# Kernel tuning notes

Measured on AMD Instinct MI355X. Metric: run time of the kernel, lower is better.

Reference implementation:

```python
import jax, jax.numpy as jnp
import numpy as np

B, T, E = 4, 2048, 768
HN, HS = 12, 64          # head_num, head_size = E // HN
L = 6                    # n_layer
FF = 4 * E
O = 1                    # output_dim
EPS = 1e-5


def setup_inputs() -> dict:
    key = jax.random.key(0)
    ks = iter(jax.random.split(key, 40))
    r = lambda shape, s=0.02: jax.random.normal(next(ks), shape, jnp.float32) * s
    inp = {
        'idx': jax.random.normal(next(ks), (B, T, E), jnp.float32),
        'hidden': jnp.zeros((1, B, E), jnp.float32),
        # per-layer, per-head q/k/v linears
        'wq': r((L, HN, E, HS)), 'bq': jnp.zeros((L, HN, HS), jnp.float32),
        'wk': r((L, HN, E, HS)), 'bk': jnp.zeros((L, HN, HS), jnp.float32),
        'wv': r((L, HN, E, HS)), 'bv': jnp.zeros((L, HN, HS), jnp.float32),
        'wproj': r((L, E, E)), 'bproj': jnp.zeros((L, E), jnp.float32),
        'ln1_g': jnp.ones((L, E), jnp.float32), 'ln1_b': jnp.zeros((L, E), jnp.float32),
        'ln2_g': jnp.ones((L, E), jnp.float32), 'ln2_b': jnp.zeros((L, E), jnp.float32),
        'w1': r((L, E, FF)), 'b1': jnp.zeros((L, FF), jnp.float32),
        'w2': r((L, FF, E)), 'b2': jnp.zeros((L, E), jnp.float32),
        'lnf_g': jnp.ones((E,), jnp.float32), 'lnf_b': jnp.zeros((E,), jnp.float32),
        'fw1': r((E, FF)), 'fb1': jnp.zeros((FF,), jnp.float32),
        'fw2': r((FF, E)), 'fb2': jnp.zeros((E,), jnp.float32),
        'hw': r((E, O)), 'hb': jnp.zeros((O,), jnp.float32),
    }
    return inp


def _layernorm(x, g, b):
    m = jnp.mean(x, axis=-1, keepdims=True)
    v = jnp.var(x, axis=-1, keepdims=True)
    return (x - m) * jax.lax.rsqrt(v + EPS) * g + b


def _forward(idx, wq, bq, wk, bk, wv, bv, wproj, bproj,
             ln1_g, ln1_b, ln2_g, ln2_b, w1, b1, w2, b2,
             lnf_g, lnf_b, fw1, fb1, fw2, fb2, hw, hb):
    x = idx
    Bn, Tn, En = x.shape
    causal = jnp.tril(jnp.ones((Tn, Tn), bool))  # [T,T]
    scale = 1.0 / jnp.sqrt(jnp.asarray(En, x.dtype))  # NOTE: divides by sqrt(n_embed), as in source
    for l in range(wq.shape[0]):
        h = _layernorm(x, ln1_g[l], ln1_b[l])
        q = jnp.einsum('bte,hes->bhts', h, wq[l]) + bq[l][None, :, None, :]
        k = jnp.einsum('bte,hes->bhts', h, wk[l]) + bk[l][None, :, None, :]
        v = jnp.einsum('bte,hes->bhts', h, wv[l]) + bv[l][None, :, None, :]
        scores = jnp.einsum('bhts,bhus->bhtu', q, k) * scale
        scores = jnp.where(causal, scores, -jnp.inf)
        att = jax.nn.softmax(scores, axis=-1)
        o = jnp.einsum('bhtu,bhus->bhts', att, v)          # [B,HN,T,HS]
        o = o.transpose(0, 2, 1, 3).reshape(Bn, Tn, En)     # concat heads
        x = x + o @ wproj[l] + bproj[l]
        h = _layernorm(x, ln2_g[l], ln2_b[l])
        ff = jax.nn.gelu(h @ w1[l] + b1[l], approximate=False) @ w2[l] + b2[l]
        x = x + ff
    x = _layernorm(x, lnf_g, lnf_b)
    x = jax.nn.gelu(x @ fw1 + fb1, approximate=False) @ fw2 + fb2
    logits = x @ hw + hb            # [B,T,O]
    logits = logits[-1]             # [T,O]  (source: logits[-1,:,:])
    return jnp.squeeze(logits, axis=-1)  # [T]


def reference(idx, hidden, wq, bq, wk, bk, wv, bv, wproj, bproj,
              ln1_g, ln1_b, ln2_g, ln2_b, w1, b1, w2, b2,
              lnf_g, lnf_b, fw1, fb1, fw2, fb2, hw, hb):
    # hidden is accepted but unused by the original module.
    del hidden
    return _forward(idx, wq, bq, wk, bk, wv, bv, wproj, bproj,
                    ln1_g, ln1_b, ln2_g, ln2_b, w1, b1, w2, b2,
                    lnf_g, lnf_b, fw1, fb1, fw2, fb2, hw, hb)
```

## Files before the change

### kernel.cpp

```cpp
#include <hip/hip_runtime.h>
#include <math.h>

#define TT 2048
#define EE 768
#define HNN 12
#define HSS 64
#define NLAYER 6
#define FFD 3072
#define QKVN 2304

constexpr float LN_EPS = 1e-5f;
constexpr float ATT_SCALE = 0.03608439182435161f;
constexpr float ATT_SCALE_L2E = 0.03608439182435161f * 1.4426950408889634f;

typedef __attribute__((ext_vector_type(8))) short bf16x8;
typedef __attribute__((ext_vector_type(4))) float f32x4;

__device__ __forceinline__ ushort f2bf(float f) {
    union { float f; uint u; } c; c.f = f;
    const uint u = c.u;
    return (ushort)((u + 0x7fffu + ((u >> 16) & 1u)) >> 16);
}

__device__ __forceinline__ void gload16(const void* g, void* l) {
    __builtin_amdgcn_global_load_lds((const __attribute__((address_space(1))) void*)g,
                                     (__attribute__((address_space(3))) void*)l, 16, 0, 0);
}

__global__ __launch_bounds__(256) void copy4_kernel(float4* __restrict__ dst,
                                                    const float4* __restrict__ src, int n4) {
    int i = blockIdx.x * 256 + threadIdx.x;
    if (i < n4) dst[i] = src[i];
}

__global__ __launch_bounds__(256) void ln_kernel(const float* __restrict__ in,
                                                 const float* __restrict__ g,
                                                 const float* __restrict__ b,
                                                 ushort* __restrict__ out) {
    __shared__ float red[8];
    const int t = blockIdx.x;
    const int tid = threadIdx.x;
    const float* row = in + (size_t)t * EE;
    float v0 = row[tid], v1 = row[tid + 256], v2 = row[tid + 512];
    float s = v0 + v1 + v2;
#pragma unroll
    for (int m = 1; m < 64; m <<= 1) s += __shfl_xor(s, m, 64);
    if ((tid & 63) == 0) red[tid >> 6] = s;
    __syncthreads();
    const float mean = (red[0] + red[1] + red[2] + red[3]) * (1.0f / EE);
    const float d0 = v0 - mean, d1 = v1 - mean, d2 = v2 - mean;
    float qq = d0 * d0 + d1 * d1 + d2 * d2;
#pragma unroll
    for (int m = 1; m < 64; m <<= 1) qq += __shfl_xor(qq, m, 64);
    __syncthreads();
    if ((tid & 63) == 0) red[tid >> 6] = qq;
    __syncthreads();
    const float var = (red[0] + red[1] + red[2] + red[3]) * (1.0f / EE);
    const float rstd = rsqrtf(var + LN_EPS);
    ushort* orow = out + (size_t)t * EE;
    orow[tid]       = f2bf(d0 * rstd * g[tid]       + b[tid]);
    orow[tid + 256] = f2bf(d1 * rstd * g[tid + 256] + b[tid + 256]);
    orow[tid + 512] = f2bf(d2 * rstd * g[tid + 512] + b[tid + 512]);
}

__device__ __forceinline__ void transpose64(const float* __restrict__ src, int sld,
                                            ushort* __restrict__ dst, int dld,
                                            int k0, int n0, int tid) {
    __shared__ float t[64][68];
#pragma unroll
    for (int p = 0; p < 4; p++) {
        const int kr = p * 16 + (tid >> 4);
        *(float4*)&t[kr][(tid & 15) * 4] =
            *(const float4*)&src[(size_t)(k0 + kr) * sld + n0 + (tid & 15) * 4];
    }
    __syncthreads();
#pragma unroll
    for (int q = 0; q < 2; q++) {
        const int nl = q * 32 + (tid >> 3);
        const int kc = (tid & 7) * 8;
        ushort v[8];
#pragma unroll
        for (int j = 0; j < 8; j++) v[j] = f2bf(t[kc + j][nl]);
        uint4 o;
        o.x = (uint)v[0] | ((uint)v[1] << 16);
        o.y = (uint)v[2] | ((uint)v[3] << 16);
        o.z = (uint)v[4] | ((uint)v[5] << 16);
        o.w = (uint)v[6] | ((uint)v[7] << 16);
        *(uint4*)&dst[(size_t)(n0 + nl) * dld + k0 + kc] = o;
    }
}

__global__ __launch_bounds__(256) void pack_t_kernel(const float* __restrict__ src, int sld,
                                                     ushort* __restrict__ dst, int dld) {
    transpose64(src, sld, dst, dld, blockIdx.x * 64, blockIdx.y * 64, threadIdx.x);
}

__global__ __launch_bounds__(256) void pack_qkv_kernel(const float* __restrict__ wq,
                                                       const float* __restrict__ wk,
                                                       const float* __restrict__ wv,
                                                       ushort* __restrict__ dst) {
    const int z = blockIdx.z;
    const int which = z / HNN, hd = z % HNN;
    const float* src = (which == 0 ? wq : which == 1 ? wk : wv) + (size_t)hd * EE * HSS;
    ushort* d = dst + (size_t)(which * EE + hd * HSS) * EE;
    transpose64(src, HSS, d, EE, blockIdx.x * 64, 0, threadIdx.x);
}

__global__ __launch_bounds__(256) void vtrans_kernel(const ushort* __restrict__ qkv,
                                                     ushort* __restrict__ vT) {
    const int t = blockIdx.x * 256 + threadIdx.x;
    const int d = t & 63;
    const int rest = t >> 6;
    const int tb = rest & 255;
    const int hd = rest >> 8;
    const ushort* src = qkv + 1536 + hd * 64 + d;
    ushort v[8];
#pragma unroll
    for (int j = 0; j < 8; j++) v[j] = src[(size_t)(tb * 8 + j) * QKVN];
    uint4 o;
    o.x = (uint)v[0] | ((uint)v[1] << 16);
    o.y = (uint)v[2] | ((uint)v[3] << 16);
    o.z = (uint)v[4] | ((uint)v[5] << 16);
    o.w = (uint)v[6] | ((uint)v[7] << 16);
    *(uint4*)&vT[((size_t)hd * 64 + d) * TT + tb * 8] = o;
}

template <int EPI>
__global__ __launch_bounds__(256) void gemm_bf16(const ushort* __restrict__ A,
                                                 const ushort* __restrict__ Bt,
                                                 const float* __restrict__ b0,
                                                 const float* __restrict__ b1,
                                                 const float* __restrict__ b2,
                                                 float* __restrict__ outF,
                                                 ushort* __restrict__ outB,
                                                 int N, int K,
                                                 int nby, int KS, int Kslice) {
    __shared__ ushort Al[2][64 * 32];
    __shared__ ushort Bl[2][128 * 32];
    const int tid = threadIdx.x;
    const int wave = tid >> 6, lane = tid & 63;
    const int l15 = lane & 15, q4 = lane >> 4;

    const int nwg = gridDim.x;
    const int wgid = ((int)blockIdx.x & 7) * (nwg >> 3) + ((int)blockIdx.x >> 3);
    const int mb = wgid % nby;
    const int t2 = wgid / nby;
    const int ks = t2 % KS;
    const int nb = t2 / KS;
    const int m0 = mb * 64, n0 = nb * 128;
    const int kbase = ks * Kslice;

    const int srow = lane >> 2;
    const int scb = (lane & 3) ^ ((lane >> 3) & 3);
    const ushort* Ag  = A + (size_t)(m0 + wave * 16 + srow) * K + kbase + scb * 8;
    const ushort* Bg0 = Bt + (size_t)(n0 + wave * 32 + srow) * K + kbase + scb * 8;
    const ushort* Bg1 = Bg0 + (size_t)16 * K;

    auto stage = [&](int buf, int kk) {
        const int off = kk * 32;
        gload16(Ag + off, &Al[buf][(wave * 16) * 32]);
        gload16(Bg0 + off, &Bl[buf][(wave * 32) * 32]);
        gload16(Bg1 + off, &Bl[buf][(wave * 32 + 16) * 32]);
    };

    f32x4 acc[4][2];
#pragma unroll
    for (int i = 0; i < 4; i++)
#pragma unroll
        for (int j = 0; j < 2; j++) acc[i][j] = (f32x4){0.f, 0.f, 0.f, 0.f};

    stage(0, 0);
    __syncthreads();

    const int niter = Kslice >> 5;
    const int cq = (q4 ^ ((l15 >> 1) & 3)) * 8;

    for (int i = 0; i < niter; i++) {
        const int buf = i & 1;
        if (i + 1 < niter) stage(buf ^ 1, i + 1);
        bf16x8 af[4], bfr[2];
#pragma unroll
        for (int ii = 0; ii < 4; ii++)
            af[ii] = *(const bf16x8*)&Al[buf][(ii * 16 + l15) * 32 + cq];
#pragma unroll
        for (int j = 0; j < 2; j++)
            bfr[j] = *(const bf16x8*)&Bl[buf][(wave * 32 + j * 16 + l15) * 32 + cq];
#pragma unroll
        for (int ii = 0; ii < 4; ii++)
#pragma unroll
            for (int j = 0; j < 2; j++)
                acc[ii][j] = __builtin_amdgcn_mfma_f32_16x16x32_bf16(af[ii], bfr[j], acc[ii][j], 0, 0, 0);
        __syncthreads();
    }

#pragma unroll
    for (int i = 0; i < 4; i++) {
        const int row = m0 + i * 16 + q4 * 4;
#pragma unroll
        for (int j = 0; j < 2; j++) {
            const int col = n0 + wave * 32 + j * 16 + l15;
            float bias;
            if constexpr (EPI == 0)
                bias = (col < 768) ? b0[col] : (col < 1536 ? b1[col - 768] : b2[col - 1536]);
            else
                bias = (EPI == 1 && ks != 0) ? 0.f : b0[col];
#pragma unroll
            for (int r = 0; r < 4; r++) {
                const float v = acc[i][j][r] + bias;
                const size_t idx = (size_t)(row + r) * N + col;
                if constexpr (EPI == 0) {
                    outB[idx] = f2bf(v);
                } else if constexpr (EPI == 1) {
                    atomicAdd(&outF[idx], v);
                } else if constexpr (EPI == 2) {
                    outB[idx] = f2bf(0.5f * v * (1.0f + erff(v * 0.70710678118654752f)));
                } else {
                    outF[idx] = v;
                }
            }
        }
    }
}

__global__ __launch_bounds__(256, 2) void attn_mfma(const ushort* __restrict__ qkv,
                                                    const ushort* __restrict__ vT,
                                                    ushort* __restrict__ o_bf) {
    __shared__ __align__(16) uint  Ps[4][16 * 36];
    __shared__ __align__(16) float Po[4][16 * 64];
    __shared__ float Pm[4][16];
    __shared__ float Pl[4][16];

    const int tid = threadIdx.x;
    const int wave = tid >> 6, lane = tid & 63;
    const int l15 = lane & 15, q4 = lane >> 4;

    const int x = (int)blockIdx.x & 7, r = (int)blockIdx.x >> 3;
    int head, qi;
    if (r < 128) { head = x;            qi = 127 - r; }
    else         { head = 8 + (x >> 1); qi = 2 * (191 - r) + (x & 1); }
    const int nkt = (qi >> 2) + 1;
    const int per = (nkt + 3) >> 2;
    const int kt0 = wave * per;
    const int kt1 = min(kt0 + per, nkt);
    const int qrow_g = qi * 16 + l15;

    const ushort* qp = qkv + (size_t)qrow_g * QKVN + head * 64;
    const bf16x8 qa0 = *(const bf16x8*)&qp[q4 * 8];
    const bf16x8 qa1 = *(const bf16x8*)&qp[32 + q4 * 8];

    const ushort* kbase = qkv + 768 + head * 64 + (size_t)l15 * QKVN + q4 * 8;
    const ushort* vbase = vT + ((size_t)head * 64 + l15) * TT + q4 * 8;

    float m_i = -1e30f, l_i = 0.f;
    f32x4 oacc[4];
#pragma unroll
    for (int n = 0; n < 4; n++) oacc[n] = (f32x4){0.f, 0.f, 0.f, 0.f};

    uint* psrow = &Ps[wave][l15 * 36];

    if (kt0 < kt1) {
        bf16x8 kA[8], kB[8], vC[8];
        {
            const ushort* kp = kbase + (size_t)kt0 * 64 * QKVN;
#pragma unroll
            for (int n = 0; n < 4; n++)
#pragma unroll
                for (int kb = 0; kb < 2; kb++)
                    kA[n * 2 + kb] = *(const bf16x8*)(kp + (size_t)(n * 16) * QKVN + kb * 32);
        }

        auto body = [&](bf16x8* kc, bf16x8* kn, int kt) {
            const ushort* vp = vbase + kt * 64;
#pragma unroll
            for (int n = 0; n < 4; n++)
#pragma unroll
                for (int kb = 0; kb < 2; kb++)
                    vC[n * 2 + kb] = *(const bf16x8*)(vp + (size_t)(n * 16) * TT + kb * 32);
            if (kt + 1 < kt1) {
                const ushort* kp = kbase + (size_t)(kt + 1) * 64 * QKVN;
#pragma unroll
                for (int n = 0; n < 4; n++)
#pragma unroll
                    for (int kb = 0; kb < 2; kb++)
                        kn[n * 2 + kb] = *(const bf16x8*)(kp + (size_t)(n * 16) * QKVN + kb * 32);
            }
            f32x4 s[4];
#pragma unroll
            for (int n = 0; n < 4; n++) {
                f32x4 a = (f32x4){0.f, 0.f, 0.f, 0.f};
                a = __builtin_amdgcn_mfma_f32_16x16x32_bf16(kc[n * 2], qa0, a, 0, 0, 0);
                a = __builtin_amdgcn_mfma_f32_16x16x32_bf16(kc[n * 2 + 1], qa1, a, 0, 0, 0);
                s[n] = a;
            }
            float pe[16];
            const bool diag = (kt == nkt - 1);
#pragma unroll
            for (int n = 0; n < 4; n++) {
                const int k0 = kt * 64 + n * 16 + q4 * 4;
#pragma unroll
                for (int rr = 0; rr < 4; rr++) {
                    float xv = s[n][rr] * ATT_SCALE_L2E;
                    if (diag && (k0 + rr) > qrow_g) xv = -1e30f;
                    pe[n * 4 + rr] = xv;
                }
            }
            float t8[8];
#pragma unroll
            for (int i = 0; i < 8; i++) t8[i] = fmaxf(pe[i], pe[i + 8]);
            float mx = fmaxf(fmaxf(fmaxf(t8[0], t8[4]), fmaxf(t8[1], t8[5])),
                             fmaxf(fmaxf(t8[2], t8[6]), fmaxf(t8[3], t8[7])));
            mx = fmaxf(mx, __shfl_xor(mx, 16, 64));
            mx = fmaxf(mx, __shfl_xor(mx, 32, 64));
            const float nm = fmaxf(m_i, mx);
            const float al = exp2f(m_i - nm);
#pragma unroll
            for (int i = 0; i < 16; i++) pe[i] = exp2f(pe[i] - nm);
            float s8[8];
#pragma unroll
            for (int i = 0; i < 8; i++) s8[i] = pe[i] + pe[i + 8];
            float rs = ((s8[0] + s8[4]) + (s8[1] + s8[5])) + ((s8[2] + s8[6]) + (s8[3] + s8[7]));
            rs += __shfl_xor(rs, 16, 64);
            rs += __shfl_xor(rs, 32, 64);
            l_i = l_i * al + rs;
            m_i = nm;
            float alr[4];
#pragma unroll
            for (int rr = 0; rr < 4; rr++) alr[rr] = __shfl(al, q4 * 4 + rr, 64);
#pragma unroll
            for (int n = 0; n < 4; n++) {
                oacc[n][0] *= alr[0];
                oacc[n][1] *= alr[1];
                oacc[n][2] *= alr[2];
                oacc[n][3] *= alr[3];
            }
#pragma unroll
            for (int n = 0; n < 4; n++) {
                uint2 d2;
                d2.x = (uint)f2bf(pe[n * 4 + 0]) | ((uint)f2bf(pe[n * 4 + 1]) << 16);
                d2.y = (uint)f2bf(pe[n * 4 + 2]) | ((uint)f2bf(pe[n * 4 + 3]) << 16);
                *(uint2*)&psrow[(8 * n + 2 * q4 + 4 * l15) & 31] = d2;
            }
            const bf16x8 pa0 = *(const bf16x8*)&psrow[(4 * q4 + 4 * l15) & 31];
            const bf16x8 pa1 = *(const bf16x8*)&psrow[(16 + 4 * q4 + 4 * l15) & 31];
#pragma unroll
            for (int n = 0; n < 4; n++) {
                oacc[n] = __builtin_amdgcn_mfma_f32_16x16x32_bf16(pa0, vC[n * 2], oacc[n], 0, 0, 0);
                oacc[n] = __builtin_amdgcn_mfma_f32_16x16x32_bf16(pa1, vC[n * 2 + 1], oacc[n], 0, 0, 0);
            }
        };

        int kt = kt0;
        for (;;) {
            body(kA, kB, kt);
            if (++kt >= kt1) break;
            body(kB, kA, kt);
            if (++kt >= kt1) break;
        }
    }

#pragma unroll
    for (int n = 0; n < 4; n++)
#pragma unroll
        for (int rr = 0; rr < 4; rr++)
            Po[wave][(q4 * 4 + rr) * 64 + n * 16 + l15] = oacc[n][rr];
    if (q4 == 0) {
        Pm[wave][l15] = m_i;
        Pl[wave][l15] = l_i;
    }
    __syncthreads();

    const int row = tid >> 4;
    const int c4 = (tid & 15) * 4;
    const float m0 = Pm[0][row], m1 = Pm[1][row], m2 = Pm[2][row], m3 = Pm[3][row];
    const float M = fmaxf(fmaxf(m0, m1), fmaxf(m2, m3));
    const float w0 = exp2f(m0 - M), w1 = exp2f(m1 - M), w2 = exp2f(m2 - M), w3 = exp2f(m3 - M);
    const float L = w0 * Pl[0][row] + w1 * Pl[1][row] + w2 * Pl[2][row] + w3 * Pl[3][row];
    const f32x4 o0 = *(const f32x4*)&Po[0][row * 64 + c4];
    const f32x4 o1 = *(const f32x4*)&Po[1][row * 64 + c4];
    const f32x4 o2 = *(const f32x4*)&Po[2][row * 64 + c4];
    const f32x4 o3 = *(const f32x4*)&Po[3][row * 64 + c4];
    const float rl = 1.0f / L;
    uint2 ow;
    {
        const float v0 = (w0 * o0[0] + w1 * o1[0] + w2 * o2[0] + w3 * o3[0]) * rl;
        const float v1 = (w0 * o0[1] + w1 * o1[1] + w2 * o2[1] + w3 * o3[1]) * rl;
        const float v2 = (w0 * o0[2] + w1 * o1[2] + w2 * o2[2] + w3 * o3[2]) * rl;
        const float v3 = (w0 * o0[3] + w1 * o1[3] + w2 * o2[3] + w3 * o3[3]) * rl;
        ow.x = (uint)f2bf(v0) | ((uint)f2bf(v1) << 16);
        ow.y = (uint)f2bf(v2) | ((uint)f2bf(v3) << 16);
    }
    *(uint2*)&o_bf[(size_t)(qi * 16 + row) * EE + head * 64 + c4] = ow;
}

__global__ __launch_bounds__(256) void head_kernel(const float* __restrict__ x,
                                                   const float* __restrict__ hw,
                                                   const float* __restrict__ hb,
                                                   float* __restrict__ out) {
    __shared__ float red[8];
    const int t = blockIdx.x, tid = threadIdx.x;
    const float* row = x + (size_t)t * EE;
    float s = row[tid] * hw[tid] + row[tid + 256] * hw[tid + 256] + row[tid + 512] * hw[tid + 512];
#pragma unroll
    for (int m = 1; m < 64; m <<= 1) s += __shfl_xor(s, m, 64);
    if ((tid & 63) == 0) red[tid >> 6] = s;
    __syncthreads();
    if (tid == 0) out[t] = red[0] + red[1] + red[2] + red[3] + hb[0];
}

extern "C" void kernel_launch(void* const* d_in, const int* in_sizes, int n_in,
                              void* d_out, int out_size, void* d_ws, size_t ws_size,
                              hipStream_t stream) {
    const float* idx   = (const float*)d_in[0];
    const float* wq    = (const float*)d_in[2];
    const float* bq    = (const float*)d_in[3];
    const float* wk    = (const float*)d_in[4];
    const float* bk    = (const float*)d_in[5];
    const float* wv    = (const float*)d_in[6];
    const float* bv    = (const float*)d_in[7];
    const float* wproj = (const float*)d_in[8];
    const float* bproj = (const float*)d_in[9];
    const float* ln1g  = (const float*)d_in[10];
    const float* ln1b  = (const float*)d_in[11];
    const float* ln2g  = (const float*)d_in[12];
    const float* ln2b  = (const float*)d_in[13];
    const float* w1    = (const float*)d_in[14];
    const float* b1    = (const float*)d_in[15];
    const float* w2    = (const float*)d_in[16];
    const float* b2    = (const float*)d_in[17];
    const float* lnfg  = (const float*)d_in[18];
    const float* lnfb  = (const float*)d_in[19];
    const float* fw1   = (const float*)d_in[20];
    const float* fb1   = (const float*)d_in[21];
    const float* fw2   = (const float*)d_in[22];
    const float* fb2   = (const float*)d_in[23];
    const float* hw    = (const float*)d_in[24];
    const float* hb    = (const float*)d_in[25];
    float* out = (float*)d_out;

    char* p = (char*)d_ws;
    auto alloc = [&](size_t bytes) { void* r = (void*)p; p += (bytes + 255) & ~(size_t)255; return r; };
    float*  x     = (float*)alloc((size_t)TT * EE * 4);
    ushort* h_bf  = (ushort*)alloc((size_t)TT * EE * 2);
    ushort* qkvb  = (ushort*)alloc((size_t)TT * QKVN * 2);
    ushort* o_bf  = (ushort*)alloc((size_t)TT * EE * 2);
    ushort* ffb   = (ushort*)alloc((size_t)TT * FFD * 2);
    ushort* Wqkv  = (ushort*)alloc((size_t)QKVN * EE * 2);
    ushort* Wproj = (ushort*)alloc((size_t)EE * EE * 2);
    ushort* W1t   = (ushort*)alloc((size_t)FFD * EE * 2);
    ushort* W2t   = (ushort*)alloc((size_t)EE * FFD * 2);
    ushort* vTb   = (ushort*)alloc((size_t)HNN * HSS * TT * 2);

    copy4_kernel<<<dim3((TT * EE / 4 + 255) / 256), dim3(256), 0, stream>>>(
        (float4*)x, (const float4*)(idx + (size_t)3 * TT * EE), TT * EE / 4);

    for (int l = 0; l < NLAYER; l++) {
        const size_t lw = (size_t)l;
        pack_qkv_kernel<<<dim3(12, 1, 36), dim3(256), 0, stream>>>(
            wq + lw * HNN * EE * HSS, wk + lw * HNN * EE * HSS, wv + lw * HNN * EE * HSS, Wqkv);
        pack_t_kernel<<<dim3(12, 12), dim3(256), 0, stream>>>(wproj + lw * EE * EE, EE, Wproj, EE);
        pack_t_kernel<<<dim3(12, 48), dim3(256), 0, stream>>>(w1 + lw * EE * FFD, FFD, W1t, EE);
        pack_t_kernel<<<dim3(48, 12), dim3(256), 0, stream>>>(w2 + lw * FFD * EE, EE, W2t, FFD);

        ln_kernel<<<dim3(TT), dim3(256), 0, stream>>>(x, ln1g + lw * EE, ln1b + lw * EE, h_bf);
        gemm_bf16<0><<<dim3(576), dim3(256), 0, stream>>>(
            h_bf, Wqkv, bq + lw * EE, bk + lw * EE, bv + lw * EE, nullptr, qkvb,
            QKVN, EE, 32, 1, EE);
        vtrans_kernel<<<dim3(768), dim3(256), 0, stream>>>(qkvb, vTb);
        attn_mfma<<<dim3(1536), dim3(256), 0, stream>>>(qkvb, vTb, o_bf);
        gemm_bf16<1><<<dim3(768), dim3(256), 0, stream>>>(
            o_bf, Wproj, bproj + lw * EE, nullptr, nullptr, x, nullptr,
            EE, EE, 32, 4, 192);
        ln_kernel<<<dim3(TT), dim3(256), 0, stream>>>(x, ln2g + lw * EE, ln2b + lw * EE, h_bf);
        gemm_bf16<2><<<dim3(768), dim3(256), 0, stream>>>(
            h_bf, W1t, b1 + lw * FFD, nullptr, nullptr, nullptr, ffb,
            FFD, EE, 32, 1, EE);
        gemm_bf16<1><<<dim3(768), dim3(256), 0, stream>>>(
            ffb, W2t, b2 + lw * EE, nullptr, nullptr, x, nullptr,
            EE, FFD, 32, 4, 768);
    }

    ln_kernel<<<dim3(TT), dim3(256), 0, stream>>>(x, lnfg, lnfb, h_bf);
    pack_t_kernel<<<dim3(12, 48), dim3(256), 0, stream>>>(fw1, FFD, W1t, EE);
    pack_t_kernel<<<dim3(48, 12), dim3(256), 0, stream>>>(fw2, EE, W2t, FFD);
    gemm_bf16<2><<<dim3(768), dim3(256), 0, stream>>>(
        h_bf, W1t, fb1, nullptr, nullptr, nullptr, ffb, FFD, EE, 32, 1, EE);
    gemm_bf16<3><<<dim3(192), dim3(256), 0, stream>>>(
        ffb, W2t, fb2, nullptr, nullptr, x, nullptr, EE, FFD, 32, 1, FFD);
    head_kernel<<<dim3(TT), dim3(256), 0, stream>>>(x, hw, hb, out);
}
```

Measured before the change: 1.442 ms.

## Assign one query tile per wave in attention, dropping split-KV merge

Attention used to split each 16-row query tile's key range across four waves, then merge their partial softmax states through shared memory after a block barrier. Now each wave owns its own 16-row query tile, and the four waves of a block share the same number of key tiles. That removes the cross-wave merge, the Po/Pm/Pl shared buffers and the __syncthreads, and the grid shrinks from 1536 to 384 blocks. V loads are now prefetched one tile ahead like K, at the cost of more registers. The risks are longer serial loops per wave, lower parallelism (384 blocks of 4 waves), and uncoalesced scalar bf16 output stores.

```diff
diff --git a/kernel.cpp b/kernel.cpp
--- a/kernel.cpp
+++ b/kernel.cpp
@@ -225,23 +225,18 @@
 __global__ __launch_bounds__(256, 2) void attn_mfma(const ushort* __restrict__ qkv,
                                                     const ushort* __restrict__ vT,
                                                     ushort* __restrict__ o_bf) {
-    __shared__ __align__(16) uint  Ps[4][16 * 36];
-    __shared__ __align__(16) float Po[4][16 * 64];
-    __shared__ float Pm[4][16];
-    __shared__ float Pl[4][16];
+    __shared__ __align__(16) uint Ps[4][16 * 36];
 
     const int tid = threadIdx.x;
     const int wave = tid >> 6, lane = tid & 63;
     const int l15 = lane & 15, q4 = lane >> 4;
 
     const int x = (int)blockIdx.x & 7, r = (int)blockIdx.x >> 3;
-    int head, qi;
-    if (r < 128) { head = x;            qi = 127 - r; }
-    else         { head = 8 + (x >> 1); qi = 2 * (191 - r) + (x & 1); }
-    const int nkt = (qi >> 2) + 1;
-    const int per = (nkt + 3) >> 2;
-    const int kt0 = wave * per;
-    const int kt1 = min(kt0 + per, nkt);
+    int head, g;
+    if (r < 32) { head = x;            g = 31 - r; }
+    else        { head = 8 + (x >> 1); g = 2 * (47 - r) + (x & 1); }
+    const int qi = g * 4 + wave;
+    const int nkt = g + 1;
     const int qrow_g = qi * 16 + l15;
 
     const ushort* qp = qkv + (size_t)qrow_g * QKVN + head * 64;
@@ -258,138 +253,109 @@
 
     uint* psrow = &Ps[wave][l15 * 36];
 
-    if (kt0 < kt1) {
-        bf16x8 kA[8], kB[8], vC[8];
-        {
-            const ushort* kp = kbase + (size_t)kt0 * 64 * QKVN;
+    bf16x8 kA[8], kB[8], vA[8], vB[8];
+#pragma unroll
+    for (int n = 0; n < 4; n++)
+#pragma unroll
+        for (int kb = 0; kb < 2; kb++) {
+            kA[n * 2 + kb] = *(const bf16x8*)(kbase + (size_t)(n * 16) * QKVN + kb * 32);
+            vA[n * 2 + kb] = *(const bf16x8*)(vbase + (size_t)(n * 16) * TT + kb * 32);
+        }
+
+    auto body = [&](bf16x8* kc, bf16x8* kn, bf16x8* vc, bf16x8* vn, int kt) {
+        if (kt + 1 < nkt) {
+            const ushort* kp = kbase + (size_t)(kt + 1) * 64 * QKVN;
+            const ushort* vp = vbase + (kt + 1) * 64;
 #pragma unroll
             for (int n = 0; n < 4; n++)
 #pragma unroll
-                for (int kb = 0; kb < 2; kb++)
-                    kA[n * 2 + kb] = *(const bf16x8*)(kp + (size_t)(n * 16) * QKVN + kb * 32);
-        }
-
-        auto body = [&](bf16x8* kc, bf16x8* kn, int kt) {
-            const ushort* vp = vbase + kt * 64;
-#pragma unroll
-            for (int n = 0; n < 4; n++)
-#pragma unroll
-                for (int kb = 0; kb < 2; kb++)
-                    vC[n * 2 + kb] = *(const bf16x8*)(vp + (size_t)(n * 16) * TT + kb * 32);
-            if (kt + 1 < kt1) {
-                const ushort* kp = kbase + (size_t)(kt + 1) * 64 * QKVN;
-#pragma unroll
-                for (int n = 0; n < 4; n++)
-#pragma unroll
-                    for (int kb = 0; kb < 2; kb++)
-                        kn[n * 2 + kb] = *(const bf16x8*)(kp + (size_t)(n * 16) * QKVN + kb * 32);
+                for (int kb = 0; kb < 2; kb++) {
+                    kn[n * 2 + kb] = *(const bf16x8*)(kp + (size_t)(n * 16) * QKVN + kb * 32);
+                    vn[n * 2 + kb] = *(const bf16x8*)(vp + (size_t)(n * 16) * TT + kb * 32);
+                }
+        }
+        f32x4 s[4];
+#pragma unroll
+        for (int n = 0; n < 4; n++) {
+            f32x4 a = (f32x4){0.f, 0.f, 0.f, 0.f};
+            a = __builtin_amdgcn_mfma_f32_16x16x32_bf16(kc[n * 2], qa0, a, 0, 0, 0);
+            a = __builtin_amdgcn_mfma_f32_16x16x32_bf16(kc[n * 2 + 1], qa1, a, 0, 0, 0);
+            s[n] = a;
+        }
+        float pe[16];
+        const bool diag = (kt == nkt - 1);
+#pragma unroll
+        for (int n = 0; n < 4; n++) {
+            const int k0 = kt * 64 + n * 16 + q4 * 4;
+#pragma unroll
+            for (int rr = 0; rr < 4; rr++) {
+                float xv = s[n][rr] * ATT_SCALE_L2E;
+                if (diag && (k0 + rr) > qrow_g) xv = -1e30f;
+                pe[n * 4 + rr] = xv;
             }
-            f32x4 s[4];
-#pragma unroll
-            for (int n = 0; n < 4; n++) {
-                f32x4 a = (f32x4){0.f, 0.f, 0.f, 0.f};
-                a = __builtin_amdgcn_mfma_f32_16x16x32_bf16(kc[n * 2], qa0, a, 0, 0, 0);
-                a = __builtin_amdgcn_mfma_f32_16x16x32_bf16(kc[n * 2 + 1], qa1, a, 0, 0, 0);
-                s[n] = a;
-            }
-            float pe[16];
-            const bool diag = (kt == nkt - 1);
-#pragma unroll
-            for (int n = 0; n < 4; n++) {
-                const int k0 = kt * 64 + n * 16 + q4 * 4;
-#pragma unroll
-                for (int rr = 0; rr < 4; rr++) {
-                    float xv = s[n][rr] * ATT_SCALE_L2E;
-                    if (diag && (k0 + rr) > qrow_g) xv = -1e30f;
-                    pe[n * 4 + rr] = xv;
-                }
-            }
-            float t8[8];
-#pragma unroll
-            for (int i = 0; i < 8; i++) t8[i] = fmaxf(pe[i], pe[i + 8]);
-            float mx = fmaxf(fmaxf(fmaxf(t8[0], t8[4]), fmaxf(t8[1], t8[5])),
-                             fmaxf(fmaxf(t8[2], t8[6]), fmaxf(t8[3], t8[7])));
-            mx = fmaxf(mx, __shfl_xor(mx, 16, 64));
-            mx = fmaxf(mx, __shfl_xor(mx, 32, 64));
-            const float nm = fmaxf(m_i, mx);
-            const float al = exp2f(m_i - nm);
-#pragma unroll
-            for (int i = 0; i < 16; i++) pe[i] = exp2f(pe[i] - nm);
-            float s8[8];
-#pragma unroll
-            for (int i = 0; i < 8; i++) s8[i] = pe[i] + pe[i + 8];
-            float rs = ((s8[0] + s8[4]) + (s8[1] + s8[5])) + ((s8[2] + s8[6]) + (s8[3] + s8[7]));
-            rs += __shfl_xor(rs, 16, 64);
-            rs += __shfl_xor(rs, 32, 64);
-            l_i = l_i * al + rs;
-            m_i = nm;
-            float alr[4];
-#pragma unroll
-            for (int rr = 0; rr < 4; rr++) alr[rr] = __shfl(al, q4 * 4 + rr, 64);
-#pragma unroll
-            for (int n = 0; n < 4; n++) {
-                oacc[n][0] *= alr[0];
-                oacc[n][1] *= alr[1];
-                oacc[n][2] *= alr[2];
-                oacc[n][3] *= alr[3];
-            }
-#pragma unroll
-            for (int n = 0; n < 4; n++) {
-                uint2 d2;
-                d2.x = (uint)f2bf(pe[n * 4 + 0]) | ((uint)f2bf(pe[n * 4 + 1]) << 16);
-                d2.y = (uint)f2bf(pe[n * 4 + 2]) | ((uint)f2bf(pe[n * 4 + 3]) << 16);
-                *(uint2*)&psrow[(8 * n + 2 * q4 + 4 * l15) & 31] = d2;
-            }
-            const bf16x8 pa0 = *(const bf16x8*)&psrow[(4 * q4 + 4 * l15) & 31];
-            const bf16x8 pa1 = *(const bf16x8*)&psrow[(16 + 4 * q4 + 4 * l15) & 31];
-#pragma unroll
-            for (int n = 0; n < 4; n++) {
-                oacc[n] = __builtin_amdgcn_mfma_f32_16x16x32_bf16(pa0, vC[n * 2], oacc[n], 0, 0, 0);
-                oacc[n] = __builtin_amdgcn_mfma_f32_16x16x32_bf16(pa1, vC[n * 2 + 1], oacc[n], 0, 0, 0);
-            }
-        };
-
-        int kt = kt0;
-        for (;;) {
-            body(kA, kB, kt);
-            if (++kt >= kt1) break;
-            body(kB, kA, kt);
-            if (++kt >= kt1) break;
-        }
-    }
-
+        }
+        float t8[8];
+#pragma unroll
+        for (int i = 0; i < 8; i++) t8[i] = fmaxf(pe[i], pe[i + 8]);
+        float mx = fmaxf(fmaxf(fmaxf(t8[0], t8[4]), fmaxf(t8[1], t8[5])),
+                         fmaxf(fmaxf(t8[2], t8[6]), fmaxf(t8[3], t8[7])));
+        mx = fmaxf(mx, __shfl_xor(mx, 16, 64));
+        mx = fmaxf(mx, __shfl_xor(mx, 32, 64));
+        const float nm = fmaxf(m_i, mx);
+        const float al = exp2f(m_i - nm);
+#pragma unroll
+        for (int i = 0; i < 16; i++) pe[i] = exp2f(pe[i] - nm);
+        float s8[8];
+#pragma unroll
+        for (int i = 0; i < 8; i++) s8[i] = pe[i] + pe[i + 8];
+        float rs = ((s8[0] + s8[4]) + (s8[1] + s8[5])) + ((s8[2] + s8[6]) + (s8[3] + s8[7]));
+        rs += __shfl_xor(rs, 16, 64);
+        rs += __shfl_xor(rs, 32, 64);
+        l_i = l_i * al + rs;
+        m_i = nm;
+        float alr[4];
+#pragma unroll
+        for (int rr = 0; rr < 4; rr++) alr[rr] = __shfl(al, q4 * 4 + rr, 64);
+#pragma unroll
+        for (int n = 0; n < 4; n++) {
+            oacc[n][0] *= alr[0];
+            oacc[n][1] *= alr[1];
+            oacc[n][2] *= alr[2];
+            oacc[n][3] *= alr[3];
+        }
+#pragma unroll
+        for (int n = 0; n < 4; n++) {
+            uint2 d2;
+            d2.x = (uint)f2bf(pe[n * 4 + 0]) | ((uint)f2bf(pe[n * 4 + 1]) << 16);
+            d2.y = (uint)f2bf(pe[n * 4 + 2]) | ((uint)f2bf(pe[n * 4 + 3]) << 16);
+            *(uint2*)&psrow[(8 * n + 2 * q4 + 4 * l15) & 31] = d2;
+        }
+        const bf16x8 pa0 = *(const bf16x8*)&psrow[(4 * q4 + 4 * l15) & 31];
+        const bf16x8 pa1 = *(const bf16x8*)&psrow[(16 + 4 * q4 + 4 * l15) & 31];
+#pragma unroll
+        for (int n = 0; n < 4; n++) {
+            oacc[n] = __builtin_amdgcn_mfma_f32_16x16x32_bf16(pa0, vc[n * 2], oacc[n], 0, 0, 0);
+            oacc[n] = __builtin_amdgcn_mfma_f32_16x16x32_bf16(pa1, vc[n * 2 + 1], oacc[n], 0, 0, 0);
+        }
+    };
+
+    int kt = 0;
+    for (;;) {
+        body(kA, kB, vA, vB, kt);
+        if (++kt >= nkt) break;
+        body(kB, kA, vB, vA, kt);
+        if (++kt >= nkt) break;
+    }
+
+    float lrec[4];
+#pragma unroll
+    for (int rr = 0; rr < 4; rr++) lrec[rr] = 1.0f / __shfl(l_i, q4 * 4 + rr, 64);
 #pragma unroll
     for (int n = 0; n < 4; n++)
 #pragma unroll
         for (int rr = 0; rr < 4; rr++)
-            Po[wave][(q4 * 4 + rr) * 64 + n * 16 + l15] = oacc[n][rr];
-    if (q4 == 0) {
-        Pm[wave][l15] = m_i;
-        Pl[wave][l15] = l_i;
-    }
-    __syncthreads();
-
-    const int row = tid >> 4;
-    const int c4 = (tid & 15) * 4;
-    const float m0 = Pm[0][row], m1 = Pm[1][row], m2 = Pm[2][row], m3 = Pm[3][row];
-    const float M = fmaxf(fmaxf(m0, m1), fmaxf(m2, m3));
-    const float w0 = exp2f(m0 - M), w1 = exp2f(m1 - M), w2 = exp2f(m2 - M), w3 = exp2f(m3 - M);
-    const float L = w0 * Pl[0][row] + w1 * Pl[1][row] + w2 * Pl[2][row] + w3 * Pl[3][row];
-    const f32x4 o0 = *(const f32x4*)&Po[0][row * 64 + c4];
-    const f32x4 o1 = *(const f32x4*)&Po[1][row * 64 + c4];
-    const f32x4 o2 = *(const f32x4*)&Po[2][row * 64 + c4];
-    const f32x4 o3 = *(const f32x4*)&Po[3][row * 64 + c4];
-    const float rl = 1.0f / L;
-    uint2 ow;
-    {
-        const float v0 = (w0 * o0[0] + w1 * o1[0] + w2 * o2[0] + w3 * o3[0]) * rl;
-        const float v1 = (w0 * o0[1] + w1 * o1[1] + w2 * o2[1] + w3 * o3[1]) * rl;
-        const float v2 = (w0 * o0[2] + w1 * o1[2] + w2 * o2[2] + w3 * o3[2]) * rl;
-        const float v3 = (w0 * o0[3] + w1 * o1[3] + w2 * o2[3] + w3 * o3[3]) * rl;
-        ow.x = (uint)f2bf(v0) | ((uint)f2bf(v1) << 16);
-        ow.y = (uint)f2bf(v2) | ((uint)f2bf(v3) << 16);
-    }
-    *(uint2*)&o_bf[(size_t)(qi * 16 + row) * EE + head * 64 + c4] = ow;
+            o_bf[(size_t)(qi * 16 + q4 * 4 + rr) * EE + head * 64 + n * 16 + l15] =
+                f2bf(oacc[n][rr] * lrec[rr]);
 }
 
 __global__ __launch_bounds__(256) void head_kernel(const float* __restrict__ x,
@@ -466,7 +432,7 @@
             h_bf, Wqkv, bq + lw * EE, bk + lw * EE, bv + lw * EE, nullptr, qkvb,
             QKVN, EE, 32, 1, EE);
         vtrans_kernel<<<dim3(768), dim3(256), 0, stream>>>(qkvb, vTb);
-        attn_mfma<<<dim3(1536), dim3(256), 0, stream>>>(qkvb, vTb, o_bf);
+        attn_mfma<<<dim3(384), dim3(256), 0, stream>>>(qkvb, vTb, o_bf);
         gemm_bf16<1><<<dim3(768), dim3(256), 0, stream>>>(
             o_bf, Wproj, bproj + lw * EE, nullptr, nullptr, x, nullptr,
             EE, EE, 32, 4, 192);
```

New measurement: 1.778 ms. +23.3%, slower.
